# Optimization experiments

Hardware: AMD Instinct MI355X
Metric: run time of the kernel (lower is better)

The kernel has to match this reference:

```python
import jax, jax.numpy as jnp
import numpy as np

HEADS = 8
HEAD_DIM = 64
SCALE = HEAD_DIM ** -0.5


def setup_inputs() -> dict:
    key = jax.random.key(0)
    k1, k2, k3 = jax.random.split(key, 3)
    b, p, n, dim = 8, 16, 256, 384
    inner = HEADS * HEAD_DIM  # 512
    x = jax.random.normal(k1, (b, p, n, dim), dtype=jnp.float32)
    w_qkv = jax.random.normal(k2, (dim, 3 * inner), dtype=jnp.float32) * (dim ** -0.5)
    w_out = jax.random.normal(k3, (inner, dim), dtype=jnp.float32) * (inner ** -0.5)
    b_out = jnp.zeros((dim,), dtype=jnp.float32)
    return {"x": x, "w_qkv": w_qkv, "w_out": w_out, "b_out": b_out}


def reference(x, w_qkv, w_out, b_out):
    b, p, n, dim = x.shape
    inner = HEADS * HEAD_DIM
    qkv = jnp.einsum('bpnd,de->bpne', x, w_qkv)  # [b,p,n,3*inner]
    q, k, v = jnp.split(qkv, 3, axis=-1)
    # [b,p,n,inner] -> [b,p,h,n,hd]
    def to_heads(t):
        return t.reshape(b, p, n, HEADS, HEAD_DIM).transpose(0, 1, 3, 2, 4)
    q, k, v = to_heads(q), to_heads(k), to_heads(v)
    dots = jnp.einsum('bphqd,bphkd->bphqk', q, k) * SCALE
    attn = jax.nn.softmax(dots, axis=-1)
    out = jnp.einsum('bphqk,bphkd->bphqd', attn, v)
    out = out.transpose(0, 1, 3, 2, 4).reshape(b, p, n, inner)
    return jnp.einsum('bpni,id->bpnd', out, w_out) + b_out
```

## Files before the change

kernel.cpp:

```cpp
#include <hip/hip_runtime.h>
#include <stdint.h>

#define DEVFN __device__ __forceinline__

typedef __attribute__((ext_vector_type(8))) __bf16 bf16x8;
typedef __attribute__((ext_vector_type(8))) short short8;
typedef __attribute__((ext_vector_type(4))) float f32x4;
typedef __attribute__((ext_vector_type(4))) unsigned int u32x4;

DEVFN unsigned short f2bf(float f) {
  union { float f; unsigned u; } v; v.f = f;
  return (unsigned short)((v.u + 0x7FFFu + ((v.u >> 16) & 1u)) >> 16);
}

DEVFN void gload_lds16(const void* g, void* l) {
  __builtin_amdgcn_global_load_lds(
      (const __attribute__((address_space(1))) void*)(uintptr_t)g,
      (__attribute__((address_space(3))) void*)(uint32_t)(uintptr_t)l,
      16, 0, 0);
}


__global__ void k_cast_x(const float* __restrict__ x, short* __restrict__ xb, int n8) {
  int i = blockIdx.x * blockDim.x + threadIdx.x;
  if (i >= n8) return;
  const f32x4* xf = (const f32x4*)x;
  f32x4 a = xf[2 * i], b = xf[2 * i + 1];
  short8 s;
  s[0] = (short)f2bf(a[0]); s[1] = (short)f2bf(a[1]);
  s[2] = (short)f2bf(a[2]); s[3] = (short)f2bf(a[3]);
  s[4] = (short)f2bf(b[0]); s[5] = (short)f2bf(b[1]);
  s[6] = (short)f2bf(b[2]); s[7] = (short)f2bf(b[3]);
  ((short8*)xb)[i] = s;
}

__global__ void k_transpose_bf(const float* __restrict__ w, short* __restrict__ wt, int R, int C) {
  int i = blockIdx.x * blockDim.x + threadIdx.x;
  if (i >= R * C) return;
  int c = i / R, r = i - c * R;
  wt[i] = (short)f2bf(w[(size_t)r * C + c]);
}


template <int BF16_OUT, int NB>
__global__ __launch_bounds__(256, NB == 8 ? 2 : 3)
void k_gemm(const short* __restrict__ A, const short* __restrict__ Bt,
            unsigned short* __restrict__ Cb, float* __restrict__ Cf,
            const float* __restrict__ bias, int M, int N, int K) {
  constexpr int BN = NB * 32;
  constexpr int BCH = NB / 2;
  __shared__ short As[3][128 * 32];
  __shared__ short Bs[3][BN * 32];
  const int tid = threadIdx.x;
  const int l = tid & 63, w = tid >> 6;
  const int ntile = N / BN;
  const int nwg = gridDim.x, cpx = nwg >> 3;
  const int bid = (blockIdx.x & 7) * cpx + (blockIdx.x >> 3);
  const int mt = bid / ntile, nt = bid % ntile;
  const int m0 = mt << 7, n0 = nt * BN;
  const int wm = (w >> 1) << 6, wn = (w & 1) * (NB * 16);

  f32x4 acc[4][NB];
#pragma unroll
  for (int i = 0; i < 4; i++)
#pragma unroll
    for (int j = 0; j < NB; j++) acc[i][j] = (f32x4){0.f, 0.f, 0.f, 0.f};

  const int nsteps = K >> 5;

  auto stage = [&](int buf, int t) {
#pragma unroll
    for (int c = 0; c < 2; ++c) {
      int ch = tid + c * 256;
      int row = ch >> 2;
      int sl = (ch & 3) ^ ((row >> 1) & 3);
      gload_lds16(A + (size_t)(m0 + row) * K + t * 32 + sl * 8, &As[buf][ch * 8]);
    }
#pragma unroll
    for (int c = 0; c < BCH; ++c) {
      int ch = tid + c * 256;
      int row = ch >> 2;
      int sl = (ch & 3) ^ ((row >> 1) & 3);
      gload_lds16(Bt + (size_t)(n0 + row) * K + t * 32 + sl * 8, &Bs[buf][ch * 8]);
    }
  };
  const int sp8 = (((l >> 4) ^ ((l >> 1) & 3)) << 3);
  auto compute = [&](int buf) {
    bf16x8 af[4], bfr[NB];
#pragma unroll
    for (int i = 0; i < 4; i++)
      af[i] = *(const bf16x8*)&As[buf][(wm + i * 16 + (l & 15)) * 32 + sp8];
#pragma unroll
    for (int j = 0; j < NB; j++)
      bfr[j] = *(const bf16x8*)&Bs[buf][(wn + j * 16 + (l & 15)) * 32 + sp8];
#pragma unroll
    for (int i = 0; i < 4; i++)
#pragma unroll
      for (int j = 0; j < NB; j++)
        acc[i][j] = __builtin_amdgcn_mfma_f32_16x16x32_bf16(af[i], bfr[j], acc[i][j], 0, 0, 0);
  };

  stage(0, 0);
  stage(1, 1);
#pragma unroll 1
  for (int t = 0; t < nsteps; ++t) {
    if (t + 1 < nsteps) {
      if constexpr (NB == 8)
        asm volatile("s_waitcnt vmcnt(6)" ::: "memory");
      else
        asm volatile("s_waitcnt vmcnt(4)" ::: "memory");
    } else {
      asm volatile("s_waitcnt vmcnt(0)" ::: "memory");
    }
    __builtin_amdgcn_sched_barrier(0);
    __builtin_amdgcn_s_barrier();
    __builtin_amdgcn_sched_barrier(0);
    if (t + 2 < nsteps) stage((t + 2) % 3, t + 2);
    compute(t % 3);
  }

#pragma unroll
  for (int i = 0; i < 4; i++) {
    int mrow = m0 + wm + i * 16 + ((l >> 4) << 2);
#pragma unroll
    for (int j = 0; j < NB; j++) {
      int ncol = n0 + wn + j * 16 + (l & 15);
#pragma unroll
      for (int r = 0; r < 4; r++) {
        if (BF16_OUT) {
          Cb[(size_t)(mrow + r) * N + ncol] = f2bf(acc[i][j][r]);
        } else {
          Cf[(size_t)(mrow + r) * N + ncol] = acc[i][j][r] + bias[ncol];
        }
      }
    }
  }
}


__global__ __launch_bounds__(512, 2)
void k_attn(const short* __restrict__ qkv, unsigned short* __restrict__ O) {
  __shared__ short Kl[256 * 64];
  __shared__ short Vt[64 * 256];

  const int tid = threadIdx.x, l = tid & 63, w = tid >> 6;
  const int g = (l >> 4) & 3;
  const int bh = blockIdx.x;
  const int bp = bh >> 3, h = bh & 7;
  const size_t tokbase = (size_t)bp * 256 * 1536;
  const int qoff = h * 64, koff = 512 + h * 64, voff = 1024 + h * 64;

#pragma unroll
  for (int c = 0; c < 4; ++c) {
    int ch = tid + c * 512;
    int row = ch >> 3, s = ch & 7;
    int sg = s ^ (row & 7);
    gload_lds16(qkv + tokbase + (size_t)row * 1536 + koff + sg * 8, &Kl[ch * 8]);
  }
#pragma unroll
  for (int c = 0; c < 4; ++c) {
    int ch = tid + c * 512;
    int row = ch >> 3, d0 = (ch & 7) * 8;
    short8 v = *(const short8*)(qkv + tokbase + (size_t)row * 1536 + voff + d0);
    int kc = row >> 5, u = row & 31;
    int gg = (u >> 2) & 3;
    int off = ((u & 16) ? 4 : 0) + (u & 3);
#pragma unroll
    for (int j = 0; j < 8; ++j) {
      int d = d0 + j;
      int sl = (kc * 4 + gg) ^ (d & 15);
      Vt[d * 256 + sl * 8 + off] = v[j];
    }
  }
  __syncthreads();

  const float CEXP = 0.125f * 1.44269504f;

#pragma unroll 1
  for (int it = 0; it < 2; ++it) {
    const int q0 = w * 32 + it * 16;
    bf16x8 qa[2];
#pragma unroll
    for (int dc = 0; dc < 2; ++dc)
      qa[dc] = *(const bf16x8*)(qkv + tokbase + (size_t)(q0 + (l & 15)) * 1536 + qoff +
                                dc * 32 + (l >> 4) * 8);
    f32x4 s[16];
#pragma unroll
    for (int kt = 0; kt < 16; kt++) s[kt] = (f32x4){0.f, 0.f, 0.f, 0.f};
#pragma unroll
    for (int dc = 0; dc < 2; ++dc) {
#pragma unroll
      for (int kt = 0; kt < 16; ++kt) {
        int kcol = kt * 16 + (l & 15);
        int sl = (dc * 4 + (l >> 4)) ^ (kcol & 7);
        bf16x8 kb = *(const bf16x8*)&Kl[kcol * 64 + sl * 8];
        s[kt] = __builtin_amdgcn_mfma_f32_16x16x32_bf16(kb, qa[dc], s[kt], 0, 0, 0);
      }
    }
    float mx = s[0][0];
#pragma unroll
    for (int kt = 0; kt < 16; kt++)
#pragma unroll
      for (int r = 0; r < 4; r++) mx = fmaxf(mx, s[kt][r]);
    mx = fmaxf(mx, __shfl_xor(mx, 16, 64));
    mx = fmaxf(mx, __shfl_xor(mx, 32, 64));

    u32x4 pa[8];
    float sum = 0.f;
#pragma unroll
    for (int kc = 0; kc < 8; ++kc) {
      float p0 = exp2f((s[2 * kc][0] - mx) * CEXP);
      float p1 = exp2f((s[2 * kc][1] - mx) * CEXP);
      float p2 = exp2f((s[2 * kc][2] - mx) * CEXP);
      float p3 = exp2f((s[2 * kc][3] - mx) * CEXP);
      float p4 = exp2f((s[2 * kc + 1][0] - mx) * CEXP);
      float p5 = exp2f((s[2 * kc + 1][1] - mx) * CEXP);
      float p6 = exp2f((s[2 * kc + 1][2] - mx) * CEXP);
      float p7 = exp2f((s[2 * kc + 1][3] - mx) * CEXP);
      sum += ((p0 + p1) + (p2 + p3)) + ((p4 + p5) + (p6 + p7));
      u32x4 pw;
      pw[0] = (unsigned)f2bf(p0) | ((unsigned)f2bf(p1) << 16);
      pw[1] = (unsigned)f2bf(p2) | ((unsigned)f2bf(p3) << 16);
      pw[2] = (unsigned)f2bf(p4) | ((unsigned)f2bf(p5) << 16);
      pw[3] = (unsigned)f2bf(p6) | ((unsigned)f2bf(p7) << 16);
      pa[kc] = pw;
    }
    sum += __shfl_xor(sum, 16, 64);
    sum += __shfl_xor(sum, 32, 64);
    float rs = 1.0f / sum;

    f32x4 o[4];
#pragma unroll
    for (int dt = 0; dt < 4; dt++) o[dt] = (f32x4){0.f, 0.f, 0.f, 0.f};
#pragma unroll
    for (int kc = 0; kc < 8; ++kc) {
      bf16x8 paf = __builtin_bit_cast(bf16x8, pa[kc]);
#pragma unroll
      for (int dt = 0; dt < 4; ++dt) {
        int d = dt * 16 + (l & 15);
        int sl = (kc * 4 + g) ^ (d & 15);
        bf16x8 vb = *(const bf16x8*)&Vt[d * 256 + sl * 8];
        o[dt] = __builtin_amdgcn_mfma_f32_16x16x32_bf16(paf, vb, o[dt], 0, 0, 0);
      }
      __builtin_amdgcn_sched_barrier(0);
    }
    float rsq[4];
#pragma unroll
    for (int r = 0; r < 4; ++r)
      rsq[r] = __shfl(rs, (l & 48) | (g * 4 + r), 64);
#pragma unroll
    for (int dt = 0; dt < 4; dt++) {
#pragma unroll
      for (int r = 0; r < 4; r++) {
        int qrow = q0 + g * 4 + r;
        int d = dt * 16 + (l & 15);
        O[(size_t)(bp * 256 + qrow) * 512 + h * 64 + d] = f2bf(o[dt][r] * rsq[r]);
      }
    }
  }
}


extern "C" void kernel_launch(void* const* d_in, const int* in_sizes, int n_in,
                              void* d_out, int out_size, void* d_ws, size_t ws_size,
                              hipStream_t stream) {
  const float* x    = (const float*)d_in[0];
  const float* wqkv = (const float*)d_in[1];
  const float* wout = (const float*)d_in[2];
  const float* bout = (const float*)d_in[3];
  float* out = (float*)d_out;
  char* ws = (char*)d_ws;

  short* Wot = (short*)(ws);
  short* Xb  = (short*)(ws + 393216);
  short* Wqt = (short*)(ws + 25559040);
  unsigned short* O = (unsigned short*)(ws + 393216);
  short* QKV = (short*)(ws + 33947648);

  k_cast_x<<<6144, 256, 0, stream>>>(x, Xb, 1572864);
  k_transpose_bf<<<2304, 256, 0, stream>>>(wqkv, Wqt, 384, 1536);
  k_transpose_bf<<<768, 256, 0, stream>>>(wout, Wot, 512, 384);
  k_gemm<1, 8><<<1536, 256, 0, stream>>>(Xb, Wqt, (unsigned short*)QKV, nullptr, nullptr,
                                         32768, 1536, 384);
  k_attn<<<1024, 512, 0, stream>>>(QKV, O);
  k_gemm<0, 4><<<768, 256, 0, stream>>>((const short*)O, Wot, nullptr, out, bout,
                                        32768, 384, 512);
  (void)in_sizes; (void)n_in; (void)out_size; (void)ws_size;
}
```

Before: 135.1 us.

## Fuse fp32-to-bf16 cast of x into the QKV projection GEMM

Removes the separate cast kernel that wrote a bf16 copy of x. The new QKV GEMM reads fp32 x directly into registers, converts it to bf16, and writes it into swizzled LDS, using a register double-buffer alongside the async LDS staging of B. This saves a full read and write pass over x, but the GEMM now reads twice as many A bytes and does the conversion work inside the main loop. That extra in-loop work could slow the pipeline.

```diff
diff --git a/kernel.cpp b/kernel.cpp
--- a/kernel.cpp
+++ b/kernel.cpp
@@ -21,24 +21,132 @@
 }
 
 
-__global__ void k_cast_x(const float* __restrict__ x, short* __restrict__ xb, int n8) {
-  int i = blockIdx.x * blockDim.x + threadIdx.x;
-  if (i >= n8) return;
-  const f32x4* xf = (const f32x4*)x;
-  f32x4 a = xf[2 * i], b = xf[2 * i + 1];
-  short8 s;
-  s[0] = (short)f2bf(a[0]); s[1] = (short)f2bf(a[1]);
-  s[2] = (short)f2bf(a[2]); s[3] = (short)f2bf(a[3]);
-  s[4] = (short)f2bf(b[0]); s[5] = (short)f2bf(b[1]);
-  s[6] = (short)f2bf(b[2]); s[7] = (short)f2bf(b[3]);
-  ((short8*)xb)[i] = s;
-}
-
 __global__ void k_transpose_bf(const float* __restrict__ w, short* __restrict__ wt, int R, int C) {
   int i = blockIdx.x * blockDim.x + threadIdx.x;
   if (i >= R * C) return;
   int c = i / R, r = i - c * R;
   wt[i] = (short)f2bf(w[(size_t)r * C + c]);
+}
+
+
+#define LOADA(A0, A1, A2, A3, T)                                             \
+  do {                                                                       \
+    const float* bA = X + (size_t)(m0 + rowA) * 384 + (T) * 32 + slA * 8;    \
+    A0 = *(const f32x4*)bA;                                                  \
+    A1 = *(const f32x4*)(bA + 4);                                            \
+    A2 = *(const f32x4*)(bA + 64 * 384);                                     \
+    A3 = *(const f32x4*)(bA + 64 * 384 + 4);                                 \
+  } while (0)
+
+#define WRITEA(BUF, A0, A1, A2, A3)                                          \
+  do {                                                                       \
+    u32x4 w0_;                                                               \
+    w0_[0] = (unsigned)f2bf(A0[0]) | ((unsigned)f2bf(A0[1]) << 16);          \
+    w0_[1] = (unsigned)f2bf(A0[2]) | ((unsigned)f2bf(A0[3]) << 16);          \
+    w0_[2] = (unsigned)f2bf(A1[0]) | ((unsigned)f2bf(A1[1]) << 16);          \
+    w0_[3] = (unsigned)f2bf(A1[2]) | ((unsigned)f2bf(A1[3]) << 16);          \
+    *(u32x4*)&As[BUF][tid * 8] = w0_;                                        \
+    u32x4 w1_;                                                               \
+    w1_[0] = (unsigned)f2bf(A2[0]) | ((unsigned)f2bf(A2[1]) << 16);          \
+    w1_[1] = (unsigned)f2bf(A2[2]) | ((unsigned)f2bf(A2[3]) << 16);          \
+    w1_[2] = (unsigned)f2bf(A3[0]) | ((unsigned)f2bf(A3[1]) << 16);          \
+    w1_[3] = (unsigned)f2bf(A3[2]) | ((unsigned)f2bf(A3[3]) << 16);          \
+    *(u32x4*)&As[BUF][(tid + 256) * 8] = w1_;                                \
+  } while (0)
+
+#define STEP_MAIN(T, C0, C1, C2, C3, N0, N1, N2, N3)                         \
+  do {                                                                       \
+    asm volatile("s_waitcnt vmcnt(4) lgkmcnt(0)" ::: "memory");              \
+    __builtin_amdgcn_sched_barrier(0);                                       \
+    __builtin_amdgcn_s_barrier();                                            \
+    __builtin_amdgcn_sched_barrier(0);                                       \
+    LOADA(N0, N1, N2, N3, (T) + 2);                                          \
+    stageB(((T) + 2) % 3, (T) + 2);                                          \
+    WRITEA(((T) + 1) % 3, C0, C1, C2, C3);                                   \
+    compute((T) % 3);                                                        \
+  } while (0)
+
+__global__ __launch_bounds__(256, 2)
+void k_gemm1(const float* __restrict__ X, const short* __restrict__ Bt,
+             unsigned short* __restrict__ Cb) {
+  __shared__ short As[3][128 * 32];
+  __shared__ short Bs[3][256 * 32];
+  const int tid = threadIdx.x, l = tid & 63, w = tid >> 6;
+  const int nwg = gridDim.x, cpx = nwg >> 3;
+  const int bid = (blockIdx.x & 7) * cpx + (blockIdx.x >> 3);
+  const int mt = bid / 6, nt = bid % 6;
+  const int m0 = mt << 7, n0 = nt * 256;
+  const int wm = (w >> 1) << 6, wn = (w & 1) * 128;
+  const int rowA = tid >> 2;
+  const int slA = (tid & 3) ^ ((rowA >> 1) & 3);
+
+  f32x4 acc[4][8];
+#pragma unroll
+  for (int i = 0; i < 4; i++)
+#pragma unroll
+    for (int j = 0; j < 8; j++) acc[i][j] = (f32x4){0.f, 0.f, 0.f, 0.f};
+
+  auto stageB = [&](int buf, int t) {
+#pragma unroll
+    for (int c = 0; c < 4; ++c) {
+      int ch = tid + c * 256;
+      int row = ch >> 2;
+      int sl = (ch & 3) ^ ((row >> 1) & 3);
+      gload_lds16(Bt + (size_t)(n0 + row) * 384 + t * 32 + sl * 8, &Bs[buf][ch * 8]);
+    }
+  };
+  const int sp8 = (((l >> 4) ^ ((l >> 1) & 3)) << 3);
+  auto compute = [&](int buf) {
+    bf16x8 af[4], bfr[8];
+#pragma unroll
+    for (int i = 0; i < 4; i++)
+      af[i] = *(const bf16x8*)&As[buf][(wm + i * 16 + (l & 15)) * 32 + sp8];
+#pragma unroll
+    for (int j = 0; j < 8; j++)
+      bfr[j] = *(const bf16x8*)&Bs[buf][(wn + j * 16 + (l & 15)) * 32 + sp8];
+#pragma unroll
+    for (int i = 0; i < 4; i++)
+#pragma unroll
+      for (int j = 0; j < 8; j++)
+        acc[i][j] = __builtin_amdgcn_mfma_f32_16x16x32_bf16(af[i], bfr[j], acc[i][j], 0, 0, 0);
+  };
+
+  f32x4 a0_, a1_, a2_, a3_, b0_, b1_, b2_, b3_;
+  LOADA(a0_, a1_, a2_, a3_, 0);
+  LOADA(b0_, b1_, b2_, b3_, 1);
+  stageB(0, 0);
+  stageB(1, 1);
+  asm volatile("s_waitcnt vmcnt(12)" ::: "memory");
+  WRITEA(0, a0_, a1_, a2_, a3_);
+
+#pragma unroll 1
+  for (int tp = 0; tp < 10; tp += 2) {
+    STEP_MAIN(tp,     b0_, b1_, b2_, b3_, a0_, a1_, a2_, a3_);
+    STEP_MAIN(tp + 1, a0_, a1_, a2_, a3_, b0_, b1_, b2_, b3_);
+  }
+  asm volatile("s_waitcnt vmcnt(4) lgkmcnt(0)" ::: "memory");
+  __builtin_amdgcn_sched_barrier(0);
+  __builtin_amdgcn_s_barrier();
+  __builtin_amdgcn_sched_barrier(0);
+  WRITEA(2, b0_, b1_, b2_, b3_);
+  compute(1);
+  asm volatile("s_waitcnt vmcnt(0) lgkmcnt(0)" ::: "memory");
+  __builtin_amdgcn_sched_barrier(0);
+  __builtin_amdgcn_s_barrier();
+  __builtin_amdgcn_sched_barrier(0);
+  compute(2);
+
+#pragma unroll
+  for (int i = 0; i < 4; i++) {
+    int mrow = m0 + wm + i * 16 + ((l >> 4) << 2);
+#pragma unroll
+    for (int j = 0; j < 8; j++) {
+      int ncol = n0 + wn + j * 16 + (l & 15);
+#pragma unroll
+      for (int r = 0; r < 4; r++)
+        Cb[(size_t)(mrow + r) * 1536 + ncol] = f2bf(acc[i][j][r]);
+    }
+  }
 }
 
 
@@ -272,16 +380,13 @@
   char* ws = (char*)d_ws;
 
   short* Wot = (short*)(ws);
-  short* Xb  = (short*)(ws + 393216);
   short* Wqt = (short*)(ws + 25559040);
   unsigned short* O = (unsigned short*)(ws + 393216);
   short* QKV = (short*)(ws + 33947648);
 
-  k_cast_x<<<6144, 256, 0, stream>>>(x, Xb, 1572864);
   k_transpose_bf<<<2304, 256, 0, stream>>>(wqkv, Wqt, 384, 1536);
   k_transpose_bf<<<768, 256, 0, stream>>>(wout, Wot, 512, 384);
-  k_gemm<1, 8><<<1536, 256, 0, stream>>>(Xb, Wqt, (unsigned short*)QKV, nullptr, nullptr,
-                                         32768, 1536, 384);
+  k_gemm1<<<1536, 256, 0, stream>>>(x, Wqt, (unsigned short*)QKV);
   k_attn<<<1024, 512, 0, stream>>>(QKV, O);
   k_gemm<0, 4><<<768, 256, 0, stream>>>((const short*)O, Wot, nullptr, out, bout,
                                         32768, 384, 512);
```

Result: faster. 130.3 us (-3.6%).
